# Kernel tuning notes

Hardware: AMD Instinct MI355X
Metric: run time of the kernel (lower is better)

## Reference

```python
import jax, jax.numpy as jnp
import numpy as np

N, F, D, M, B, K = 100000, 256, 128, 10, 32768, 32


def setup_inputs() -> dict:
    key = jax.random.key(0)
    ks = jax.random.split(key, 14)
    stdv = float(1.0 / np.sqrt(D))
    inp = {
        "feature": jax.random.normal(ks[0], (N, F), jnp.float32),
        "flow_char_adj": jax.random.uniform(ks[1], (M, N), jnp.float32),
        "history": jax.random.randint(ks[2], (B, K), 0, N),
        "item_id": jax.random.randint(ks[3], (B,), 0, N),
        "category_r": jax.random.randint(ks[4], (B,), 0, 2),
        "category_n": jax.random.randint(ks[5], (B,), 0, 2),
        "PA_level": jax.random.randint(ks[6], (B,), 0, M),
        # learned parameters (uniform(-stdv, stdv) as in reset_parameters)
        "weight_emb": jax.random.uniform(ks[7], (F, D), jnp.float32, -stdv, stdv),
        "bias_emb": jax.random.uniform(ks[8], (D,), jnp.float32, -stdv, stdv),
        "weight_character": jax.random.uniform(ks[9], (2 * D, D), jnp.float32, -stdv, stdv),
        "att1_w": jax.random.uniform(ks[10], (D, 1), jnp.float32, -stdv, stdv),
        "att1_b": jax.random.uniform(ks[11], (1,), jnp.float32, -stdv, stdv),
        "linear1_w": jax.random.uniform(ks[12], (2 * D, D), jnp.float32, -stdv, stdv),
        "linear1_b": jax.random.uniform(ks[13], (D,), jnp.float32, -stdv, stdv),
    }
    return inp


def reference(feature, flow_char_adj, weight_emb, bias_emb, weight_character,
              att1_w, att1_b, linear1_w, linear1_b,
              history, item_id, category_r, category_n, PA_level):
    # embedding_encode
    flow_emb = feature @ weight_emb + bias_emb              # [N, D]
    character_emb = flow_char_adj @ flow_emb                # [M, D] (spmm)

    # character_modeling (shared for r and n)
    def char_lat(cat, pa):
        ce = jnp.concatenate([character_emb[cat], character_emb[pa]], axis=1)  # [B, 2D]
        return jax.nn.sigmoid(ce @ weight_character)        # [B, D]

    lat_r = char_lat(category_r, PA_level)
    lat_n = char_lat(category_n, PA_level)

    # attribute_agg: mix flow emb with its 2 category embeddings
    flow_all = (flow_emb + flow_char_adj[:2].T @ character_emb[:2]) * 0.5  # [N, D]

    # Flow_Aggregator: per-node neighbor attention (batched over ragged lists,
    # here padded to fixed degree K)
    neigh = flow_all[history]                                # [B, K, D]
    scores = neigh @ att1_w + att1_b                         # [B, K, 1]
    att = jax.nn.softmax(scores, axis=1)                     # softmax over neighbors
    agg = jnp.sum(att * neigh, axis=1)                       # [B, D]

    # NOTE: in the torch source, self_flow_latent is mutated in-place so
    # self_feats aliases neigh_feats -> both halves of the concat equal agg.
    combined = jnp.concatenate([agg, agg], axis=1)           # [B, 2D]
    out = jax.nn.relu(combined @ linear1_w + linear1_b)      # [B, D] (dropout p=0)

    pred_r = jnp.sum(lat_r * out, axis=1)                    # [B]
    pred_n = jnp.sum(lat_n * out, axis=1)                    # [B]
    return pred_r, pred_n
```

## Files before the change

kernel.cpp:

```cpp
#include <hip/hip_runtime.h>
#include <cmath>

#define NN 100000
#define FF 256
#define DDIM 128
#define MM 10
#define BB 32768
#define KK 32
#define NB1 1563
#define NREP 64

#define OFF_Q     0
#define OFF_CEREP 100096
#define OFF_CE    182016
#define OFF_LAT   183296
#define OFF_CE01  185856
#define OFF_CS    186112
#define OFF_AGGB  186128
#define OFF_FE8   2283280
#define OFF_WF    5483280
#define OFF_WPF   5499664

typedef __attribute__((ext_vector_type(8))) short bf16x8;
typedef __attribute__((ext_vector_type(4))) float floatx4;
typedef __attribute__((ext_vector_type(2))) float floatx2;

__device__ __forceinline__ unsigned short f2bf(float x) {
  union { float f; unsigned u; } v; v.f = x;
  unsigned r = v.u + 0x7FFFu + ((v.u >> 16) & 1u);
  return (unsigned short)(r >> 16);
}

__device__ __forceinline__ bf16x8 cvt8(float4 a, float4 b) {
  short h[8];
  h[0] = (short)f2bf(a.x); h[1] = (short)f2bf(a.y);
  h[2] = (short)f2bf(a.z); h[3] = (short)f2bf(a.w);
  h[4] = (short)f2bf(b.x); h[5] = (short)f2bf(b.y);
  h[6] = (short)f2bf(b.z); h[7] = (short)f2bf(b.w);
  return *reinterpret_cast<bf16x8*>(h);
}

__device__ __forceinline__ void gload_lds16(const float* g, void* l) {
  __builtin_amdgcn_global_load_lds(
      (const __attribute__((address_space(1))) void*)g,
      (__attribute__((address_space(3))) void*)l, 16, 0, 0);
}

__global__ __launch_bounds__(256) void k0_wprep(const float* __restrict__ wemb,
                                                const float* __restrict__ l1w,
                                                short* __restrict__ wf,
                                                short* __restrict__ wpf)
{
  const int t = blockIdx.x * 256 + threadIdx.x;
  if (t < 4096) {
    const int kk = t >> 9, rem = t & 511;
    const int ct = rem >> 6, l = rem & 63;
    const int n = ct * 16 + (l & 15);
    const int kbase = kk * 32 + (l >> 4) * 8;
    short hi[8];
#pragma unroll
    for (int j = 0; j < 8; j++) hi[j] = (short)f2bf(wemb[(kbase + j) * 128 + n]);
    *reinterpret_cast<int4*>(&wf[((kk * 8 + ct) * 64 + l) * 8]) = *reinterpret_cast<int4*>(hi);
  } else {
    const int t2 = t - 4096;
    const int kk = t2 >> 9, rem = t2 & 511;
    const int ct = rem >> 6, l = rem & 63;
    const int n = ct * 16 + (l & 15);
    short h[8];
#pragma unroll
    for (int j = 0; j < 8; j++) {
      const int kp = kk * 32 + (l >> 4) * 8 + j;
      const int i = ((kp & 7) << 4) | (kp >> 3);
      h[j] = (short)f2bf(l1w[i * 128 + n] + l1w[(128 + i) * 128 + n]);
    }
    *reinterpret_cast<int4*>(&wpf[((kk * 8 + ct) * 64 + l) * 8]) = *reinterpret_cast<int4*>(h);
  }
}

__global__ __launch_bounds__(256, 2) void k1_fused(const float* __restrict__ feat,
    const short* __restrict__ wf, const float* __restrict__ bemb,
    const float* __restrict__ attw, const float* __restrict__ adj,
    float* __restrict__ q, unsigned char* __restrict__ fe8,
    float* __restrict__ cerep)
{
  __shared__ __align__(16) unsigned char ldsraw[65536];
  const int tid = threadIdx.x;
  const int wv = tid >> 6, l = tid & 63;
  const int lane16 = l & 15, quad = l >> 4;
  const int rowbase = blockIdx.x * 64;

  int r = rowbase + wv * 16 + lane16;
  if (r > NN - 1) r = NN - 1;
  const float* gp = &feat[(size_t)r * 256 + (l >> 4) * 4];
  unsigned char* wbase = ldsraw + wv * 16384;
#pragma unroll
  for (int i = 0; i < 16; i++)
    gload_lds16(gp + i * 16, wbase + i * 1024);
  __builtin_amdgcn_s_waitcnt(0);

  floatx4 acc[8];
#pragma unroll
  for (int ct = 0; ct < 8; ct++) acc[ct] = floatx4{0.f, 0.f, 0.f, 0.f};

#pragma unroll
  for (int kk = 0; kk < 8; kk++) {
    const float4 f0 = *reinterpret_cast<const float4*>(
        wbase + kk * 2048 + quad * 512 + lane16 * 16);
    const float4 f1 = *reinterpret_cast<const float4*>(
        wbase + kk * 2048 + quad * 512 + lane16 * 16 + 256);
    const bf16x8 a = cvt8(f0, f1);
    const short* wb = &wf[kk * 4096 + l * 8];
#pragma unroll
    for (int ct = 0; ct < 8; ct++) {
      const bf16x8 bh = *reinterpret_cast<const bf16x8*>(&wb[ct * 512]);
      acc[ct] = __builtin_amdgcn_mfma_f32_16x16x32_bf16(a, bh, acc[ct], 0, 0, 0);
    }
  }

  float bembv[8], attwv[8];
#pragma unroll
  for (int ct = 0; ct < 8; ct++) {
    bembv[ct] = bemb[ct * 16 + lane16];
    attwv[ct] = attw[ct * 16 + lane16];
  }
#pragma unroll
  for (int reg = 0; reg < 4; reg++) {
    const int rr = rowbase + wv * 16 + quad * 4 + reg;
    float v[8]; float qp = 0.f;
#pragma unroll
    for (int ct = 0; ct < 8; ct++) {
      v[ct] = acc[ct][reg] + bembv[ct];
      qp = fmaf(v[ct], attwv[ct], qp);
    }
    acc[0][reg] = v[0]; acc[1][reg] = v[1]; acc[2][reg] = v[2]; acc[3][reg] = v[3];
    acc[4][reg] = v[4]; acc[5][reg] = v[5]; acc[6][reg] = v[6]; acc[7][reg] = v[7];
    qp += __shfl_xor(qp, 1, 16);
    qp += __shfl_xor(qp, 2, 16);
    qp += __shfl_xor(qp, 4, 16);
    qp += __shfl_xor(qp, 8, 16);
    if (rr < NN) {
      unsigned u0 = __builtin_amdgcn_cvt_pk_fp8_f32(v[0], v[1], 0, false);
      u0 = __builtin_amdgcn_cvt_pk_fp8_f32(v[2], v[3], u0, true);
      unsigned u1 = __builtin_amdgcn_cvt_pk_fp8_f32(v[4], v[5], 0, false);
      u1 = __builtin_amdgcn_cvt_pk_fp8_f32(v[6], v[7], u1, true);
      *reinterpret_cast<uint2*>(&fe8[(size_t)rr * 128 + lane16 * 8]) = make_uint2(u0, u1);
      if (lane16 == 0) q[rr] = 0.5f * qp;
    }
  }

  __syncthreads();
#pragma unroll
  for (int rp = 0; rp < 2; rp++) {
    const int rloc = wv * 16 + quad * 4 + rp * 2;
    const int g0 = rowbase + rloc;
#pragma unroll
    for (int ct = 0; ct < 8; ct++) {
      const unsigned short h0 = (g0     < NN) ? f2bf(acc[ct][rp * 2])     : (unsigned short)0;
      const unsigned short h1 = (g0 + 1 < NN) ? f2bf(acc[ct][rp * 2 + 1]) : (unsigned short)0;
      const unsigned pk = (unsigned)h0 | ((unsigned)h1 << 16);
      *reinterpret_cast<unsigned*>(&ldsraw[(ct * 16 + lane16) * 144 + rloc * 2]) = pk;
    }
  }
  __syncthreads();

  floatx4 cacc[2];
  cacc[0] = floatx4{0.f, 0.f, 0.f, 0.f};
  cacc[1] = floatx4{0.f, 0.f, 0.f, 0.f};
  const int mclamp = (lane16 < 10) ? lane16 : 9;
#pragma unroll
  for (int kc = 0; kc < 2; kc++) {
    int n0 = rowbase + kc * 32 + quad * 8;
    if (n0 > NN - 8) n0 = NN - 8;
    const float4 f0 = *reinterpret_cast<const float4*>(&adj[(size_t)mclamp * NN + n0]);
    const float4 f1 = *reinterpret_cast<const float4*>(&adj[(size_t)mclamp * NN + n0 + 4]);
    const bf16x8 afr = cvt8(f0, f1);
#pragma unroll
    for (int tt = 0; tt < 2; tt++) {
      const int col = (wv * 2 + tt) * 16 + lane16;
      const bf16x8 bfr = *reinterpret_cast<const bf16x8*>(
          &ldsraw[col * 144 + (kc * 32 + quad * 8) * 2]);
      cacc[tt] = __builtin_amdgcn_mfma_f32_16x16x32_bf16(afr, bfr, cacc[tt], 0, 0, 0);
    }
  }
  float* myrep = &cerep[(blockIdx.x & (NREP - 1)) * 1280];
#pragma unroll
  for (int tt = 0; tt < 2; tt++) {
#pragma unroll
    for (int reg = 0; reg < 4; reg++) {
      const int m = quad * 4 + reg;
      if (m < 10)
        atomicAdd(&myrep[m * 128 + (wv * 2 + tt) * 16 + lane16], cacc[tt][reg]);
    }
  }
}

__global__ __launch_bounds__(256) void k3r_reduce(const float* __restrict__ cerep,
                                                  float* __restrict__ ce)
{
  const int o = blockIdx.x * 256 + threadIdx.x;
  if (o < 1280) {
    float s = 0.f;
#pragma unroll 8
    for (int r = 0; r < NREP; r++) s += cerep[r * 1280 + o];
    ce[o] = s;
  }
}

__global__ __launch_bounds__(128) void k3_prep(const float* __restrict__ ce,
    const float* __restrict__ wchar, const float* __restrict__ attw,
    float* __restrict__ latTab, float* __restrict__ ce01p, float* __restrict__ cs)
{
  const int blk = blockIdx.x, tid = threadIdx.x;
  __shared__ float cec[128], cep[128];
  if (blk < 20) {
    const int c = blk / 10, p = blk % 10;
    cec[tid] = ce[c * 128 + tid];
    cep[tid] = ce[p * 128 + tid];
    __syncthreads();
    float s = 0.f;
#pragma unroll 4
    for (int j = 0; j < 128; j++) {
      s = fmaf(cec[j], wchar[j * 128 + tid], s);
      s = fmaf(cep[j], wchar[(128 + j) * 128 + tid], s);
    }
    latTab[blk * 128 + tid] = 1.f / (1.f + expf(-s));
  } else {
    const float s0 = ce[tid];
    const float s1 = ce[128 + tid];
    const int pidx = (tid & 15) * 8 + (tid >> 4);
    ce01p[pidx] = s0;
    ce01p[128 + pidx] = s1;
    cec[tid] = s0 * attw[tid];
    cep[tid] = s1 * attw[tid];
    __syncthreads();
    if (tid < 64) {
      float p0 = cec[tid] + cec[tid + 64];
      float p1 = cep[tid] + cep[tid + 64];
#pragma unroll
      for (int off = 32; off >= 1; off >>= 1) {
        p0 += __shfl_xor(p0, off);
        p1 += __shfl_xor(p1, off);
      }
      if (tid == 0) { cs[0] = 0.5f * p0; cs[1] = 0.5f * p1; }
    }
  }
}

__global__ __launch_bounds__(256) void k4a_attn(const unsigned char* __restrict__ fe8,
    const float* __restrict__ q, const float* __restrict__ adj,
    const int* __restrict__ history, const float* __restrict__ cs,
    const float* __restrict__ attb_p, const float* __restrict__ ce01p,
    short* __restrict__ aggb)
{
  const int tid = threadIdx.x;
  const int lane = tid & 63;
  const int wv = tid >> 6;
  const int half = lane >> 5;
  const int t = lane & 31;
  const int b = blockIdx.x * 8 + wv * 2 + half;

  const int n_my = history[b * 32 + t];
  const float a0 = adj[n_my];
  const float a1 = adj[NN + n_my];
  const float sc = q[n_my] + a0 * cs[0] + a1 * cs[1] + attb_p[0];
  float m = sc;
#pragma unroll
  for (int off = 16; off >= 1; off >>= 1) m = fmaxf(m, __shfl_xor(m, off, 32));
  const float e = expf(sc - m);
  float sum = e;
#pragma unroll
  for (int off = 16; off >= 1; off >>= 1) sum += __shfl_xor(sum, off, 32);
  const float att = e / sum;
  float p0 = att * a0, p1 = att * a1;
#pragma unroll
  for (int off = 16; off >= 1; off >>= 1) {
    p0 += __shfl_xor(p0, off, 32);
    p1 += __shfl_xor(p1, off, 32);
  }

  float4 acc = make_float4(0.f, 0.f, 0.f, 0.f);
#pragma unroll
  for (int k = 0; k < 32; k++) {
    const int nk = __shfl(n_my, k, 32);
    const float ak = __shfl(att, k, 32);
    const unsigned u = *reinterpret_cast<const unsigned*>(&fe8[(size_t)nk * 128 + t * 4]);
    const floatx2 lo = __builtin_amdgcn_cvt_pk_f32_fp8(u, false);
    const floatx2 hi = __builtin_amdgcn_cvt_pk_f32_fp8(u, true);
    acc.x = fmaf(ak, lo[0], acc.x);
    acc.y = fmaf(ak, lo[1], acc.y);
    acc.z = fmaf(ak, hi[0], acc.z);
    acc.w = fmaf(ak, hi[1], acc.w);
  }
  const int col = t * 4;
  const float4 c0 = *reinterpret_cast<const float4*>(&ce01p[col]);
  const float4 c1 = *reinterpret_cast<const float4*>(&ce01p[128 + col]);
  const float ox = 0.5f * (acc.x + p0 * c0.x + p1 * c1.x);
  const float oy = 0.5f * (acc.y + p0 * c0.y + p1 * c1.y);
  const float oz = 0.5f * (acc.z + p0 * c0.z + p1 * c1.z);
  const float ow = 0.5f * (acc.w + p0 * c0.w + p1 * c1.w);
  const unsigned lo_ = (unsigned)f2bf(ox) | ((unsigned)f2bf(oy) << 16);
  const unsigned hi_ = (unsigned)f2bf(oz) | ((unsigned)f2bf(ow) << 16);
  *reinterpret_cast<uint2*>(&aggb[(size_t)b * 128 + col]) = make_uint2(lo_, hi_);
}

__global__ __launch_bounds__(256) void k4b_mfma(const short* __restrict__ aggb,
    const short* __restrict__ wpf, const float* __restrict__ l1b,
    const float* __restrict__ latTab,
    const int* __restrict__ cr, const int* __restrict__ cn, const int* __restrict__ pa,
    float* __restrict__ out)
{
  const int tid = threadIdx.x;
  const int wv = tid >> 6, l = tid & 63;
  const int lane16 = l & 15, quad = l >> 4;
  const int rowbase = blockIdx.x * 128 + wv * 32;
  const int r0 = rowbase + lane16;
  const int r1 = r0 + 16;

  floatx4 acc[2][8];
#pragma unroll
  for (int rt = 0; rt < 2; rt++)
#pragma unroll
    for (int ct = 0; ct < 8; ct++) acc[rt][ct] = floatx4{0.f, 0.f, 0.f, 0.f};

#pragma unroll
  for (int kk = 0; kk < 4; kk++) {
    const bf16x8 a0 = *reinterpret_cast<const bf16x8*>(&aggb[(size_t)r0 * 128 + kk * 32 + quad * 8]);
    const bf16x8 a1 = *reinterpret_cast<const bf16x8*>(&aggb[(size_t)r1 * 128 + kk * 32 + quad * 8]);
    const short* wb = &wpf[kk * 4096 + l * 8];
#pragma unroll
    for (int ct = 0; ct < 8; ct++) {
      const bf16x8 bh = *reinterpret_cast<const bf16x8*>(&wb[ct * 512]);
      acc[0][ct] = __builtin_amdgcn_mfma_f32_16x16x32_bf16(a0, bh, acc[0][ct], 0, 0, 0);
      acc[1][ct] = __builtin_amdgcn_mfma_f32_16x16x32_bf16(a1, bh, acc[1][ct], 0, 0, 0);
    }
  }

  float bb[8];
#pragma unroll
  for (int ct = 0; ct < 8; ct++) bb[ct] = l1b[ct * 16 + lane16];
#pragma unroll
  for (int rt = 0; rt < 2; rt++) {
#pragma unroll
    for (int reg = 0; reg < 4; reg++) {
      const int r = rowbase + rt * 16 + quad * 4 + reg;
      const int ir  = (cr[r] * 10 + pa[r]) * 128;
      const int in_ = (cn[r] * 10 + pa[r]) * 128;
      float pr = 0.f, pn = 0.f;
#pragma unroll
      for (int ct = 0; ct < 8; ct++) {
        const float v = fmaxf(acc[rt][ct][reg] + bb[ct], 0.f);
        pr = fmaf(v, latTab[ir  + ct * 16 + lane16], pr);
        pn = fmaf(v, latTab[in_ + ct * 16 + lane16], pn);
      }
      pr += __shfl_xor(pr, 1, 16); pr += __shfl_xor(pr, 2, 16);
      pr += __shfl_xor(pr, 4, 16); pr += __shfl_xor(pr, 8, 16);
      pn += __shfl_xor(pn, 1, 16); pn += __shfl_xor(pn, 2, 16);
      pn += __shfl_xor(pn, 4, 16); pn += __shfl_xor(pn, 8, 16);
      if (lane16 == 0) { out[r] = pr; out[BB + r] = pn; }
    }
  }
}

extern "C" void kernel_launch(void* const* d_in, const int* in_sizes, int n_in,
                              void* d_out, int out_size, void* d_ws, size_t ws_size,
                              hipStream_t stream) {
  const float* feat  = (const float*)d_in[0];
  const float* adj   = (const float*)d_in[1];
  const int*   hist  = (const int*)d_in[2];
  const int*   cr    = (const int*)d_in[4];
  const int*   cn    = (const int*)d_in[5];
  const int*   pa    = (const int*)d_in[6];
  const float* wemb  = (const float*)d_in[7];
  const float* bemb  = (const float*)d_in[8];
  const float* wchar = (const float*)d_in[9];
  const float* attw  = (const float*)d_in[10];
  const float* attb  = (const float*)d_in[11];
  const float* l1w   = (const float*)d_in[12];
  const float* l1b   = (const float*)d_in[13];
  float* out = (float*)d_out;
  float* ws  = (float*)d_ws;

  float* q     = ws + OFF_Q;
  float* cerep = ws + OFF_CEREP;
  float* ce    = ws + OFF_CE;
  float* lat   = ws + OFF_LAT;
  float* ce01p = ws + OFF_CE01;
  float* cs    = ws + OFF_CS;
  short* aggb  = (short*)(ws + OFF_AGGB);
  unsigned char* fe8 = (unsigned char*)(ws + OFF_FE8);
  short* wf    = (short*)(ws + OFF_WF);
  short* wpf   = (short*)(ws + OFF_WPF);

  hipMemsetAsync(cerep, 0, NREP * 1280 * sizeof(float), stream);
  k0_wprep<<<24, 256, 0, stream>>>(wemb, l1w, wf, wpf);
  k1_fused<<<NB1, 256, 0, stream>>>(feat, wf, bemb, attw, adj, q, fe8, cerep);
  k3r_reduce<<<5, 256, 0, stream>>>(cerep, ce);
  k3_prep<<<21, 128, 0, stream>>>(ce, wchar, attw, lat, ce01p, cs);
  k4a_attn<<<4096, 256, 0, stream>>>(fe8, q, adj, hist, cs, attb, ce01p, aggb);
  k4b_mfma<<<256, 256, 0, stream>>>(aggb, wpf, l1b, lat, cr, cn, pa, out);
}
```

Before: 281.2 us.

## Precompute bf16 MFMA A-fragments of features in a separate kernel

Adds a kernel that converts the fp32 feature matrix into bf16 MFMA A-fragment layout in a workspace buffer. The main embedding kernel then loads those fragments directly instead of staging fp32 rows through 64 KB of LDS. This cuts the fused kernel's LDS use to allow higher occupancy and removes in-kernel conversion. The cost is an extra global round trip of the converted features and one more kernel launch.

```diff
diff --git a/kernel.cpp b/kernel.cpp
--- a/kernel.cpp
+++ b/kernel.cpp
@@ -20,6 +20,7 @@
 #define OFF_FE8   2283280
 #define OFF_WF    5483280
 #define OFF_WPF   5499664
+#define OFF_AF    5507856
 
 typedef __attribute__((ext_vector_type(8))) short bf16x8;
 typedef __attribute__((ext_vector_type(4))) float floatx4;
@@ -38,12 +39,6 @@
   h[4] = (short)f2bf(b.x); h[5] = (short)f2bf(b.y);
   h[6] = (short)f2bf(b.z); h[7] = (short)f2bf(b.w);
   return *reinterpret_cast<bf16x8*>(h);
-}
-
-__device__ __forceinline__ void gload_lds16(const float* g, void* l) {
-  __builtin_amdgcn_global_load_lds(
-      (const __attribute__((address_space(1))) void*)g,
-      (__attribute__((address_space(3))) void*)l, 16, 0, 0);
 }
 
 __global__ __launch_bounds__(256) void k0_wprep(const float* __restrict__ wemb,
@@ -77,26 +72,54 @@
   }
 }
 
-__global__ __launch_bounds__(256, 2) void k1_fused(const float* __restrict__ feat,
+__global__ __launch_bounds__(256) void kW_afrag(const float* __restrict__ feat,
+                                                short* __restrict__ af)
+{
+  __shared__ __align__(16) float4 tile[16 * 65];
+  const int tid = threadIdx.x;
+  const int rowbase = blockIdx.x * 64;
+#pragma unroll 1
+  for (int g = 0; g < 4; g++) {
+    if (g) __syncthreads();
+#pragma unroll
+    for (int i = 0; i < 4; i++) {
+      const int idx = i * 256 + tid;
+      const int r16 = idx >> 6, f4 = idx & 63;
+      int gr = rowbase + g * 16 + r16; if (gr > NN - 1) gr = NN - 1;
+      tile[r16 * 65 + f4] = *reinterpret_cast<const float4*>(&feat[(size_t)gr * 256 + f4 * 4]);
+    }
+    __syncthreads();
+#pragma unroll
+    for (int i = 0; i < 2; i++) {
+      const int item = i * 256 + tid;
+      const int kk = item >> 6, lane = item & 63;
+      const int lane16 = lane & 15, quad = lane >> 4;
+      const float4 f0 = tile[lane16 * 65 + kk * 8 + quad * 2];
+      const float4 f1 = tile[lane16 * 65 + kk * 8 + quad * 2 + 1];
+      const bf16x8 a = cvt8(f0, f1);
+      *reinterpret_cast<bf16x8*>(
+          &af[(((size_t)blockIdx.x * 4 + g) * 8 + kk) * 512 + lane * 8]) = a;
+    }
+  }
+}
+
+__global__ __launch_bounds__(256) void k1_fused(const short* __restrict__ af,
     const short* __restrict__ wf, const float* __restrict__ bemb,
     const float* __restrict__ attw, const float* __restrict__ adj,
     float* __restrict__ q, unsigned char* __restrict__ fe8,
     float* __restrict__ cerep)
 {
-  __shared__ __align__(16) unsigned char ldsraw[65536];
+  __shared__ __align__(16) unsigned char cetile[128 * 144];
   const int tid = threadIdx.x;
   const int wv = tid >> 6, l = tid & 63;
   const int lane16 = l & 15, quad = l >> 4;
   const int rowbase = blockIdx.x * 64;
 
-  int r = rowbase + wv * 16 + lane16;
-  if (r > NN - 1) r = NN - 1;
-  const float* gp = &feat[(size_t)r * 256 + (l >> 4) * 4];
-  unsigned char* wbase = ldsraw + wv * 16384;
-#pragma unroll
-  for (int i = 0; i < 16; i++)
-    gload_lds16(gp + i * 16, wbase + i * 1024);
-  __builtin_amdgcn_s_waitcnt(0);
+  const short* afb = &af[(((size_t)blockIdx.x * 4 + wv) * 8) * 512 + l * 8];
+  bf16x8 afr[8];
+#pragma unroll
+  for (int kk = 0; kk < 8; kk++)
+    afr[kk] = *reinterpret_cast<const bf16x8*>(&afb[kk * 512]);
 
   floatx4 acc[8];
 #pragma unroll
@@ -104,16 +127,11 @@
 
 #pragma unroll
   for (int kk = 0; kk < 8; kk++) {
-    const float4 f0 = *reinterpret_cast<const float4*>(
-        wbase + kk * 2048 + quad * 512 + lane16 * 16);
-    const float4 f1 = *reinterpret_cast<const float4*>(
-        wbase + kk * 2048 + quad * 512 + lane16 * 16 + 256);
-    const bf16x8 a = cvt8(f0, f1);
     const short* wb = &wf[kk * 4096 + l * 8];
 #pragma unroll
     for (int ct = 0; ct < 8; ct++) {
       const bf16x8 bh = *reinterpret_cast<const bf16x8*>(&wb[ct * 512]);
-      acc[ct] = __builtin_amdgcn_mfma_f32_16x16x32_bf16(a, bh, acc[ct], 0, 0, 0);
+      acc[ct] = __builtin_amdgcn_mfma_f32_16x16x32_bf16(afr[kk], bh, acc[ct], 0, 0, 0);
     }
   }
 
@@ -148,7 +166,6 @@
     }
   }
 
-  __syncthreads();
 #pragma unroll
   for (int rp = 0; rp < 2; rp++) {
     const int rloc = wv * 16 + quad * 4 + rp * 2;
@@ -158,7 +175,7 @@
       const unsigned short h0 = (g0     < NN) ? f2bf(acc[ct][rp * 2])     : (unsigned short)0;
       const unsigned short h1 = (g0 + 1 < NN) ? f2bf(acc[ct][rp * 2 + 1]) : (unsigned short)0;
       const unsigned pk = (unsigned)h0 | ((unsigned)h1 << 16);
-      *reinterpret_cast<unsigned*>(&ldsraw[(ct * 16 + lane16) * 144 + rloc * 2]) = pk;
+      *reinterpret_cast<unsigned*>(&cetile[(ct * 16 + lane16) * 144 + rloc * 2]) = pk;
     }
   }
   __syncthreads();
@@ -173,13 +190,13 @@
     if (n0 > NN - 8) n0 = NN - 8;
     const float4 f0 = *reinterpret_cast<const float4*>(&adj[(size_t)mclamp * NN + n0]);
     const float4 f1 = *reinterpret_cast<const float4*>(&adj[(size_t)mclamp * NN + n0 + 4]);
-    const bf16x8 afr = cvt8(f0, f1);
+    const bf16x8 afr2 = cvt8(f0, f1);
 #pragma unroll
     for (int tt = 0; tt < 2; tt++) {
       const int col = (wv * 2 + tt) * 16 + lane16;
       const bf16x8 bfr = *reinterpret_cast<const bf16x8*>(
-          &ldsraw[col * 144 + (kc * 32 + quad * 8) * 2]);
-      cacc[tt] = __builtin_amdgcn_mfma_f32_16x16x32_bf16(afr, bfr, cacc[tt], 0, 0, 0);
+          &cetile[col * 144 + (kc * 32 + quad * 8) * 2]);
+      cacc[tt] = __builtin_amdgcn_mfma_f32_16x16x32_bf16(afr2, bfr, cacc[tt], 0, 0, 0);
     }
   }
   float* myrep = &cerep[(blockIdx.x & (NREP - 1)) * 1280];
@@ -390,10 +407,12 @@
   unsigned char* fe8 = (unsigned char*)(ws + OFF_FE8);
   short* wf    = (short*)(ws + OFF_WF);
   short* wpf   = (short*)(ws + OFF_WPF);
+  short* af    = (short*)(ws + OFF_AF);
 
   hipMemsetAsync(cerep, 0, NREP * 1280 * sizeof(float), stream);
   k0_wprep<<<24, 256, 0, stream>>>(wemb, l1w, wf, wpf);
-  k1_fused<<<NB1, 256, 0, stream>>>(feat, wf, bemb, attw, adj, q, fe8, cerep);
+  kW_afrag<<<NB1, 256, 0, stream>>>(feat, af);
+  k1_fused<<<NB1, 256, 0, stream>>>(af, wf, bemb, attw, adj, q, fe8, cerep);
   k3r_reduce<<<5, 256, 0, stream>>>(cerep, ce);
   k3_prep<<<21, 128, 0, stream>>>(ce, wchar, attw, lat, ce01p, cs);
   k4a_attn<<<4096, 256, 0, stream>>>(fe8, q, adj, hist, cs, attb, ce01p, aggb);
```

Measured after the change: 288.5 us. +2.6%, slower.
